# Kernel optimization log

Hardware: AMD Instinct MI355X
Metric: run time of the kernel (lower is better)

## Reference

```python
import jax, jax.numpy as jnp
import numpy as np

IO = 1024
D_SLOT = 128
SCALES = [1, 2, 4]
N = 4          # lcm of scales (streams / period)
K = 3          # number of scales (active slots per step)
S = 7          # sum of scales (total slots)
D = D_SLOT * S # 896, per-stream dim
H = K * N      # 12 heads
RANK = 256
HID = 3584
B, T = 4, 1024
EPS = 1e-5


def _tables():
    # active_slots[phase, scale_idx] -> slot id
    act = np.zeros((N, K), dtype=np.int32)
    for p in range(N):
        off = 0
        for i, s in enumerate(SCALES):
            act[p, i] = off + p % s
            off += s
    # head_assignments[stream, slot] -> head id (SHARED mode)
    ha = np.zeros((N, S), dtype=np.int32)
    off = 0
    for i, s in enumerate(SCALES):
        alpha = N // s
        for j in range(s):
            ha[:, off + j] = i * N + (np.arange(N) + alpha * j) % N
        off += s
    return act, ha

ACTIVE_SLOTS, HEAD_ASSIGN = _tables()


def layernorm(x, g, b):
    m = jnp.mean(x, axis=-1, keepdims=True)
    v = jnp.mean(jnp.square(x - m), axis=-1, keepdims=True)
    return (x - m) * jax.lax.rsqrt(v + EPS) * g + b


def setup_inputs() -> dict:
    key = jax.random.key(0)
    ks = jax.random.split(key, 16)
    f32 = jnp.float32
    return {
        'x': jax.random.normal(ks[0], (B, T, IO), f32),
        't': 3,
        'enc_base_w': jax.random.normal(ks[1], (D, IO), f32) * 0.02,
        'enc_A_w': jax.random.normal(ks[2], (RANK, IO), f32) * 0.02,
        'enc_B': jax.random.normal(ks[3], (RANK, N, D), f32) * 0.02,
        'enc_beta': jnp.asarray(0.01, f32),
        'ln_mixer_g': jnp.ones((D,), f32),
        'ln_mixer_b': jnp.zeros((D,), f32),
        'mix_w1': jax.random.normal(ks[4], (HID, D), f32) * 0.02,
        'mix_b1': jnp.zeros((HID,), f32),
        'mix_w2': jax.random.normal(ks[5], (D, HID), f32) * 0.02,
        'mix_b2': jnp.zeros((D,), f32),
        'ln_attn_g': jnp.ones((D,), f32),
        'ln_attn_b': jnp.zeros((D,), f32),
        'Wq': jax.random.normal(ks[6], (H, D, D_SLOT), f32) * 0.02,
        'Wk': jax.random.normal(ks[7], (H, D, D_SLOT), f32) * 0.02,
        'Wv': jax.random.normal(ks[8], (H, D, D_SLOT), f32) * 0.02,
        'dec_ln_g': jnp.ones((N * D,), f32),
        'dec_ln_b': jnp.zeros((N * D,), f32),
        'dec_down_w': jax.random.normal(ks[9], (RANK, N * D), f32) * 0.02,
        'dec_up_w': jax.random.normal(ks[10], (IO, RANK), f32) * 0.02,
    }


def reference(x, t, enc_base_w, enc_A_w, enc_B, enc_beta,
              ln_mixer_g, ln_mixer_b, mix_w1, mix_b1, mix_w2, mix_b2,
              ln_attn_g, ln_attn_b, Wq, Wk, Wv,
              dec_ln_g, dec_ln_b, dec_down_w, dec_up_w):
    b, tt, _ = x.shape
    # --- StreamLoRAEncoder: x [B,T,IO] -> z [B,T,N,D] ---
    base = x @ enc_base_w.T                       # [B,T,D]
    h = x @ enc_A_w.T                             # [B,T,RANK]
    delta = jnp.einsum('btr,rnd->btnd', h, enc_B) # [B,T,N,D]
    z = base[:, :, None, :] + enc_beta * delta

    # --- step(z, t, is_causal=True) ---
    phase = int(t) % N
    active = ACTIVE_SLOTS[phase]                               # [K]
    head_ids = HEAD_ASSIGN[np.arange(N)[:, None], active[None, :]]  # [N,K]

    # mixer (pre-LN MLP residual)
    zm = layernorm(z, ln_mixer_g, ln_mixer_b)
    m = jax.nn.gelu(zm @ mix_w1.T + mix_b1, approximate=False) @ mix_w2.T + mix_b2
    z_head = z + m                                             # [B,T,N,D]

    # per-head multi-scale attention; head input scope = STREAM (full D)
    hin = layernorm(z_head, ln_attn_g, ln_attn_b)              # [B,T,N,D]
    Wq_s, Wk_s, Wv_s = Wq[head_ids], Wk[head_ids], Wv[head_ids]  # [N,K,D,d]
    q = jnp.einsum('btnc,nkcd->btnkd', hin, Wq_s)
    k = jnp.einsum('btnc,nkcd->btnkd', hin, Wk_s)
    v = jnp.einsum('btnc,nkcd->btnkd', hin, Wv_s)
    scale = 1.0 / jnp.sqrt(jnp.asarray(D_SLOT, q.dtype))
    scores = jnp.einsum('bqnkd,bpnkd->bnkqp', q, k) * scale    # [B,N,K,T,T]
    causal = jnp.tril(jnp.ones((tt, tt), dtype=bool))
    scores = jnp.where(causal, scores, jnp.finfo(scores.dtype).min)
    attn = jax.nn.softmax(scores, axis=-1)
    out = jnp.einsum('bnkqp,bpnkd->bqnkd', attn, v)            # [B,T,N,K,d]

    # write attention outputs back into the active slots (residual)
    z_slots = z_head.reshape(b, tt, N, S, D_SLOT)
    z_new = z_slots.at[:, :, :, jnp.asarray(active), :].add(out)
    z_new = z_new.reshape(b, tt, N, D)

    # --- StreamLoRADecoder: z [B,T,N,D] -> y [B,T,IO] ---
    cat = z_new.reshape(b, tt, N * D)
    c = layernorm(cat, dec_ln_g, dec_ln_b)
    y = (c @ dec_down_w.T) @ dec_up_w.T
    return y
```

## Files before the change

### kernel.cpp

```cpp
#include <hip/hip_runtime.h>
#include <hip/hip_bf16.h>
#include <math.h>

typedef __hip_bfloat16 bf16;
typedef __attribute__((ext_vector_type(8))) short v8s;
typedef __attribute__((ext_vector_type(4))) float v4f;

#define EPI_F32    0
#define EPI_BF16   1
#define EPI_GELU   2
#define EPI_RESID  3
#define EPI_BCAST4 4
#define EPI_AXPY   5
#define EPI_RESID0 6

__device__ __forceinline__ float bf_lo(unsigned int w) { return __uint_as_float(w << 16); }
__device__ __forceinline__ float bf_hi(unsigned int w) { return __uint_as_float(w & 0xffff0000u); }
__device__ __forceinline__ unsigned short f2b_bits(float f) {
  unsigned int u = __float_as_uint(f);
  unsigned int r = (u + 0x7fffu + ((u >> 16) & 1u)) >> 16;
  return (unsigned short)r;
}
__device__ __forceinline__ void unpack8(uint4 u, float* f) {
  unsigned int w0 = u.x, w1 = u.y, w2 = u.z, w3 = u.w;
  f[0] = bf_lo(w0); f[1] = bf_hi(w0);
  f[2] = bf_lo(w1); f[3] = bf_hi(w1);
  f[4] = bf_lo(w2); f[5] = bf_hi(w2);
  f[6] = bf_lo(w3); f[7] = bf_hi(w3);
}
__device__ __forceinline__ void load8(const float* p, float* f) {
  float4 a = ((const float4*)p)[0];
  float4 b = ((const float4*)p)[1];
  f[0] = a.x; f[1] = a.y; f[2] = a.z; f[3] = a.w;
  f[4] = b.x; f[5] = b.y; f[6] = b.z; f[7] = b.w;
}
__device__ __forceinline__ void gl_lds16(const void* g, void* l) {
  __builtin_amdgcn_global_load_lds(
      (__attribute__((address_space(1))) void*)g,
      (__attribute__((address_space(3))) void*)l, 16, 0, 0);
}

__global__ __launch_bounds__(256) void cvt_kernel(const float* __restrict__ src,
                                                  bf16* __restrict__ dst, int n)
{
  int i = (blockIdx.x * 256 + threadIdx.x) * 8;
  if (i >= n) return;
  float f[8]; load8(src + i, f);
  unsigned short us[8];
#pragma unroll
  for (int j = 0; j < 8; j++) us[j] = f2b_bits(f[j]);
  *(uint4*)((unsigned short*)dst + i) = *(uint4*)us;
}

__global__ __launch_bounds__(256) void cvt_t_kernel(const float* __restrict__ src,
                                                    bf16* __restrict__ dst, int R, int C)
{
  __shared__ float tile[32][33];
  const int c0 = blockIdx.x * 32, r0 = blockIdx.y * 32;
  const size_t bo = (size_t)blockIdx.z * R * C;
  const int tx = threadIdx.x & 31, ty = threadIdx.x >> 5;
#pragma unroll
  for (int i = 0; i < 4; i++) {
    int r = ty * 4 + i;
    tile[r][tx] = src[bo + (size_t)(r0 + r) * C + c0 + tx];
  }
  __syncthreads();
#pragma unroll
  for (int i = 0; i < 4; i++) {
    int r = ty * 4 + i;
    *((unsigned short*)dst + bo + (size_t)(c0 + r) * R + r0 + tx) = f2b_bits(tile[tx][r]);
  }
}

__global__ __launch_bounds__(256) void vt_kernel(const bf16* __restrict__ v,
                                                 bf16* __restrict__ vt)
{
  __shared__ float tile[64][65];
  const int h = blockIdx.z;
  const int t0 = blockIdx.x * 64, d0 = blockIdx.y * 64;
  const bf16* src = v + (size_t)h * 4096 * 128;
  bf16* dst = vt + (size_t)h * 128 * 4096;
  const int tid = threadIdx.x;
#pragma unroll
  for (int tt = 0; tt < 2; tt++) {
    int s = tt * 256 + tid;
    int r = s >> 3, c0 = (s & 7) * 8;
    float f[8];
    uint4 u = *(const uint4*)(src + (size_t)(t0 + r) * 128 + d0 + c0);
    unpack8(u, f);
#pragma unroll
    for (int j = 0; j < 8; j++) tile[r][c0 + j] = f[j];
  }
  __syncthreads();
#pragma unroll
  for (int tt = 0; tt < 2; tt++) {
    int s = tt * 256 + tid;
    int dr = s >> 3, c0 = (s & 7) * 8;
    unsigned short us[8];
#pragma unroll
    for (int j = 0; j < 8; j++) us[j] = f2b_bits(tile[c0 + j][dr]);
    *(uint4*)((unsigned short*)dst + (size_t)(d0 + dr) * 4096 + t0 + c0) = *(uint4*)us;
  }
}

__device__ __forceinline__ void stage_async(const bf16* __restrict__ src, int ld, int r0, int k0,
                                            bf16* lds, int wave, int lane)
{
#pragma unroll
  for (int t = 0; t < 2; t++) {
    int seg = wave * 2 + t;
    const bf16* g = src + (size_t)(r0 + seg * 16 + (lane >> 2)) * ld + k0 + (lane & 3) * 8;
    gl_lds16(g, lds + seg * 512);
  }
}
__device__ __forceinline__ void stage_sync(const float* __restrict__ src, int ld, int r0, int k0,
                                           bf16* lds, int tid)
{
#pragma unroll
  for (int t = 0; t < 2; t++) {
    int s = t * 256 + tid;
    int m = s >> 2, c = s & 3;
    float f[8]; load8(src + (size_t)(r0 + m) * ld + k0 + c * 8, f);
    unsigned short us[8];
#pragma unroll
    for (int j = 0; j < 8; j++) us[j] = f2b_bits(f[j]);
    *(uint4*)&lds[m * 32 + c * 8] = *(uint4*)us;
  }
}
__device__ __forceinline__ void stage_tile(const bf16* __restrict__ src, int ld, int r0, int k0,
                                           bf16* lds, int tid, int wave, int lane)
{ stage_async(src, ld, r0, k0, lds, wave, lane); }
__device__ __forceinline__ void stage_tile(const float* __restrict__ src, int ld, int r0, int k0,
                                           bf16* lds, int tid, int wave, int lane)
{ stage_sync(src, ld, r0, k0, lds, tid); }

template<typename TA, typename TB, int EPI>
__device__ void mfma_core(const TA* __restrict__ A, int lda,
                          const TB* __restrict__ B, int ldb,
                          void* __restrict__ C, int ldc,
                          const float* __restrict__ bias,
                          const float* __restrict__ beta_p,
                          int m0, int n0, int K)
{
  __shared__ bf16 As[128 * 32];
  __shared__ bf16 Bs[128 * 32];
  const int tid = threadIdx.x;
  const int lane = tid & 63, wave = tid >> 6;
  const int mw = (wave & 1) * 64, nw = (wave >> 1) * 64;
  const int row = lane & 15, kc = lane >> 4;

  v4f acc[4][4];
  const v4f vzero = {0.f, 0.f, 0.f, 0.f};
#pragma unroll
  for (int i = 0; i < 4; i++)
#pragma unroll
    for (int j = 0; j < 4; j++) acc[i][j] = vzero;

  for (int k0 = 0; k0 < K; k0 += 32) {
    stage_tile(A, lda, m0, k0, As, tid, wave, lane);
    stage_tile(B, ldb, n0, k0, Bs, tid, wave, lane);
    __syncthreads();
    v8s af[4], bfr[4];
#pragma unroll
    for (int i = 0; i < 4; i++)
      af[i] = *(const v8s*)&As[(mw + i * 16 + row) * 32 + kc * 8];
#pragma unroll
    for (int j = 0; j < 4; j++)
      bfr[j] = *(const v8s*)&Bs[(nw + j * 16 + row) * 32 + kc * 8];
#pragma unroll
    for (int i = 0; i < 4; i++)
#pragma unroll
      for (int j = 0; j < 4; j++)
        acc[i][j] = __builtin_amdgcn_mfma_f32_16x16x32_bf16(af[i], bfr[j], acc[i][j], 0, 0, 0);
    __syncthreads();
  }

  const int cl = lane & 15, rq = lane >> 4;
  const float beta = (EPI == EPI_AXPY) ? beta_p[0] : 0.f;
#pragma unroll
  for (int mi = 0; mi < 4; mi++) {
#pragma unroll
    for (int nj = 0; nj < 4; nj++) {
      const int col = n0 + nw + nj * 16 + cl;
#pragma unroll
      for (int i = 0; i < 4; i++) {
        const int r = m0 + mw + mi * 16 + rq * 4 + i;
        float v = acc[mi][nj][i];
        if (EPI == EPI_F32) {
          ((float*)C)[(size_t)r * ldc + col] = v;
        } else if (EPI == EPI_BF16) {
          ((unsigned short*)C)[(size_t)r * ldc + col] = f2b_bits(v);
        } else if (EPI == EPI_GELU) {
          v += bias[col];
          v = 0.5f * v * (1.f + erff(v * 0.70710678118654752f));
          ((unsigned short*)C)[(size_t)r * ldc + col] = f2b_bits(v);
        } else if (EPI == EPI_RESID) {
          float* Z = (float*)C;
          size_t idx = (size_t)r * ldc + col;
          Z[idx] = Z[idx] + v + bias[col];
        } else if (EPI == EPI_RESID0) {
          float* Z = (float*)C;
          size_t idx = (size_t)r * ldc + col;
          Z[idx] = Z[idx] + v;
        } else if (EPI == EPI_BCAST4) {
          float* Z = (float*)C;
#pragma unroll
          for (int rep = 0; rep < 4; rep++)
            Z[(size_t)r * 3584 + rep * 896 + col] = v;
        } else if (EPI == EPI_AXPY) {
          float* Z = (float*)C;
          size_t idx = (size_t)r * 3584 + col;
          Z[idx] = Z[idx] + beta * v;
        }
      }
    }
  }
}

template<typename TA, typename TB, int EPI>
__global__ __launch_bounds__(256) void mfma_gemm(const TA* __restrict__ A, int lda,
                                                 const TB* __restrict__ B, int ldb,
                                                 void* __restrict__ C, int ldc,
                                                 const float* __restrict__ bias,
                                                 const float* __restrict__ beta_p, int K)
{
  mfma_core<TA, TB, EPI>(A, lda, B, ldb, C, ldc, bias, beta_p,
                         blockIdx.y * 128, blockIdx.x * 128, K);
}

template<typename TA, typename TB, int EPI>
__global__ __launch_bounds__(256) void mfma_gemm_sw(const TA* __restrict__ A, int lda,
                                                    const TB* __restrict__ B, int ldb,
                                                    void* __restrict__ C, int ldc,
                                                    const float* __restrict__ bias,
                                                    const float* __restrict__ beta_p, int K)
{
  const int lin = blockIdx.x;
  const int m0 = ((((lin & 7) << 4) | ((lin >> 3) & 15))) * 128;
  const int n0 = (lin >> 7) * 128;
  mfma_core<TA, TB, EPI>(A, lda, B, ldb, C, ldc, bias, beta_p, m0, n0, K);
}

__global__ __launch_bounds__(256) void qkv_mfma(const bf16* __restrict__ hin,
                                                const bf16* __restrict__ Wt,
                                                bf16* __restrict__ qkv,
                                                const int* __restrict__ tptr)
{
  const int zb = blockIdx.z;
  const int type = zb / 12, rem = zb % 12, n = rem / 3, kh = rem % 3;
  const int phase = ((tptr[0] % 4) + 4) % 4;
  const int hid = (kh == 0) ? n
                : (kh == 1) ? 4 + (n + 2 * (phase & 1)) % 4
                            : 8 + (n + phase) % 4;
  const bf16* B = Wt + ((size_t)type * 12 + hid) * 128 * 896;
  bf16* out = qkv + ((size_t)type * 12 + n * 3 + kh) * 4096 * 128;
  mfma_core<bf16, bf16, EPI_BF16>(hin + n * 896, 3584, B, 896, out, 128,
                                  nullptr, nullptr, blockIdx.y * 128, 0, 896);
}

__global__ __launch_bounds__(256) void ln_kernel(const float* __restrict__ in,
                                                 const float* __restrict__ g,
                                                 const float* __restrict__ bsh,
                                                 bf16* __restrict__ out, int D)
{
  __shared__ float row[3584];
  __shared__ float red[256];
  const int tid = threadIdx.x;
  const size_t base = (size_t)blockIdx.x * D;
  float s = 0.f;
  for (int i = tid; i < D; i += 256) { float v = in[base + i]; row[i] = v; s += v; }
  red[tid] = s; __syncthreads();
  for (int o = 128; o > 0; o >>= 1) { if (tid < o) red[tid] += red[tid + o]; __syncthreads(); }
  const float mean = red[0] / (float)D;
  __syncthreads();
  s = 0.f;
  for (int i = tid; i < D; i += 256) { float d = row[i] - mean; s += d * d; }
  red[tid] = s; __syncthreads();
  for (int o = 128; o > 0; o >>= 1) { if (tid < o) red[tid] += red[tid + o]; __syncthreads(); }
  const float inv = rsqrtf(red[0] / (float)D + 1e-5f);
  for (int i = tid; i < D; i += 256) {
    float v = (row[i] - mean) * inv * g[i] + bsh[i];
    *((unsigned short*)out + base + i) = f2b_bits(v);
  }
}

__global__ __launch_bounds__(256) void attn_mfma(const bf16* __restrict__ qkv,
                                                 const bf16* __restrict__ vt,
                                                 float* __restrict__ z,
                                                 const int* __restrict__ tptr)
{
  __shared__ bf16 Ks[64 * 136];
  __shared__ bf16 Vs[128 * 72];
  __shared__ bf16 Ps[4][16 * 72];
  const int tid = threadIdx.x;
  const int lane = tid & 63, wave = tid >> 6;
  const int cl = lane & 15, rq = lane >> 4;
  const int qb = 15 - blockIdx.x;
  const int bnk = blockIdx.y;
  const int b = bnk / 12, rem = bnk % 12, n = rem / 3, kh = rem % 3;
  const int phase = ((tptr[0] % 4) + 4) % 4;
  const int slot = (kh == 0) ? 0 : (kh == 1) ? 1 + (phase & 1) : 3 + phase;
  const int head = n * 3 + kh;
  const size_t HS = (size_t)12 * 4096 * 128;
  const bf16* qp = qkv + ((size_t)head * 4096 + b * 1024) * 128;
  const bf16* kp = qkv + HS + ((size_t)head * 4096 + b * 1024) * 128;
  const bf16* vtp = vt + (size_t)head * 128 * 4096;

  v8s aq[4];
  {
    const bf16* qrow = qp + (size_t)(qb * 64 + wave * 16 + cl) * 128 + rq * 8;
#pragma unroll
    for (int c = 0; c < 4; c++) aq[c] = *(const v8s*)(qrow + c * 32);
  }
  v4f oacc[8];
  const v4f vzero = {0.f, 0.f, 0.f, 0.f};
#pragma unroll
  for (int c = 0; c < 8; c++) oacc[c] = vzero;
  float m_i[4] = {-1e30f, -1e30f, -1e30f, -1e30f};
  float l_i[4] = {0.f, 0.f, 0.f, 0.f};

  for (int kt = 0; kt <= qb; kt++) {
    __syncthreads();
#pragma unroll
    for (int t = 0; t < 4; t++) {
      int s = t * 256 + tid;
      int r = s >> 4, c0 = (s & 15) * 8;
      *(uint4*)&Ks[r * 136 + c0] = *(const uint4*)(kp + (size_t)(kt * 64 + r) * 128 + c0);
    }
#pragma unroll
    for (int t = 0; t < 4; t++) {
      int s = t * 256 + tid;
      int d = s >> 3, c0 = (s & 7) * 8;
      *(uint4*)&Vs[d * 72 + c0] =
          *(const uint4*)(vtp + (size_t)d * 4096 + b * 1024 + kt * 64 + c0);
    }
    __syncthreads();

    v4f s_acc[4];
#pragma unroll
    for (int blk = 0; blk < 4; blk++) {
      s_acc[blk] = vzero;
#pragma unroll
      for (int c = 0; c < 4; c++) {
        v8s bk = *(const v8s*)&Ks[(blk * 16 + cl) * 136 + c * 32 + rq * 8];
        s_acc[blk] = __builtin_amdgcn_mfma_f32_16x16x32_bf16(aq[c], bk, s_acc[blk], 0, 0, 0);
      }
    }
#pragma unroll
    for (int blk = 0; blk < 4; blk++)
#pragma unroll
      for (int i = 0; i < 4; i++) {
        float sv = s_acc[blk][i] * 0.088388347648318447f;
        if (kt == qb && (blk * 16 + cl) > (wave * 16 + rq * 4 + i)) sv = -1e30f;
        s_acc[blk][i] = sv;
      }
    float al[4];
#pragma unroll
    for (int i = 0; i < 4; i++) {
      float mx = fmaxf(fmaxf(s_acc[0][i], s_acc[1][i]), fmaxf(s_acc[2][i], s_acc[3][i]));
      mx = fmaxf(mx, __shfl_xor(mx, 1, 64));
      mx = fmaxf(mx, __shfl_xor(mx, 2, 64));
      mx = fmaxf(mx, __shfl_xor(mx, 4, 64));
      mx = fmaxf(mx, __shfl_xor(mx, 8, 64));
      const float mn = fmaxf(m_i[i], mx);
      al[i] = __expf(m_i[i] - mn);
      m_i[i] = mn;
      float ps = 0.f;
#pragma unroll
      for (int blk = 0; blk < 4; blk++) {
        float p = __expf(s_acc[blk][i] - mn);
        s_acc[blk][i] = p;
        ps += p;
      }
      ps += __shfl_xor(ps, 1, 64);
      ps += __shfl_xor(ps, 2, 64);
      ps += __shfl_xor(ps, 4, 64);
      ps += __shfl_xor(ps, 8, 64);
      l_i[i] = l_i[i] * al[i] + ps;
    }
#pragma unroll
    for (int c = 0; c < 8; c++)
#pragma unroll
      for (int i = 0; i < 4; i++) oacc[c][i] *= al[i];
    bf16* ps = Ps[wave];
#pragma unroll
    for (int blk = 0; blk < 4; blk++)
#pragma unroll
      for (int i = 0; i < 4; i++)
        *((unsigned short*)ps + (rq * 4 + i) * 72 + blk * 16 + cl) = f2b_bits(s_acc[blk][i]);
    v8s pa[2];
#pragma unroll
    for (int c = 0; c < 2; c++)
      pa[c] = *(const v8s*)&ps[cl * 72 + c * 32 + rq * 8];
#pragma unroll
    for (int c = 0; c < 8; c++)
#pragma unroll
      for (int ch = 0; ch < 2; ch++) {
        v8s bv = *(const v8s*)&Vs[(c * 16 + cl) * 72 + ch * 32 + rq * 8];
        oacc[c] = __builtin_amdgcn_mfma_f32_16x16x32_bf16(pa[ch], bv, oacc[c], 0, 0, 0);
      }
  }
#pragma unroll
  for (int c = 0; c < 8; c++) {
    const int d = c * 16 + cl;
#pragma unroll
    for (int i = 0; i < 4; i++) {
      const int t = qb * 64 + wave * 16 + rq * 4 + i;
      float* dst = z + ((size_t)(b * 1024 + t)) * 3584 + n * 896 + slot * 128 + d;
      *dst += oacc[c][i] / l_i[i];
    }
  }
}

extern "C" void kernel_launch(void* const* d_in, const int* in_sizes, int n_in,
                              void* d_out, int out_size, void* d_ws, size_t ws_size,
                              hipStream_t stream)
{
  const float* x        = (const float*)d_in[0];
  const int*   tptr     = (const int*)d_in[1];
  const float* enc_base = (const float*)d_in[2];
  const float* enc_A    = (const float*)d_in[3];
  const float* enc_B    = (const float*)d_in[4];
  const float* beta_p   = (const float*)d_in[5];
  const float* lnm_g    = (const float*)d_in[6];
  const float* lnm_b    = (const float*)d_in[7];
  const float* w1       = (const float*)d_in[8];
  const float* b1       = (const float*)d_in[9];
  const float* w2       = (const float*)d_in[10];
  const float* b2       = (const float*)d_in[11];
  const float* lna_g    = (const float*)d_in[12];
  const float* lna_b    = (const float*)d_in[13];
  const float* Wq       = (const float*)d_in[14];
  const float* Wk       = (const float*)d_in[15];
  const float* Wv       = (const float*)d_in[16];
  const float* dln_g    = (const float*)d_in[17];
  const float* dln_b    = (const float*)d_in[18];
  const float* down_w   = (const float*)d_in[19];
  const float* up_w     = (const float*)d_in[20];

  const bool big = (ws_size >= (size_t)228458496);
  char* ws = (char*)d_ws;
  float* z = (float*)ws;
  bf16 *hbuf, *act, *qkv, *bufb, *w1b, *w2b, *encBt, *Wt;
  if (big) {
    hbuf  = (bf16*)(ws + (size_t)58720256);
    act   = (bf16*)(ws + (size_t)58720256);
    qkv   = (bf16*)(ws + (size_t)58720256);
    bufb  = (bf16*)(ws + (size_t)176160768);
    w1b   = (bf16*)(ws + (size_t)205520896);
    w2b   = (bf16*)(ws + (size_t)211943424);
    encBt = (bf16*)(ws + (size_t)218365952);
    Wt    = (bf16*)(ws + (size_t)220200960);
  } else {
    hbuf  = (bf16*)(ws + (size_t)58720256);
    act   = (bf16*)(ws + (size_t)58720256);
    qkv   = (bf16*)(ws + (size_t)58720256);
    bufb  = (bf16*)(ws + (size_t)96468992);
    w1b   = (bf16*)(ws + (size_t)125829120);
    w2b   = (bf16*)(ws + (size_t)132251648);
    encBt = (bf16*)(ws + (size_t)138674176);
    Wt    = (bf16*)(ws + (size_t)140509184);
  }

  dim3 blk(256);
  cvt_kernel<<<1568, blk, 0, stream>>>(w1, w1b, 3211264);
  cvt_kernel<<<1568, blk, 0, stream>>>(w2, w2b, 3211264);
  cvt_t_kernel<<<dim3(112, 8, 1), blk, 0, stream>>>(enc_B, encBt, 256, 3584);
  cvt_t_kernel<<<dim3(4, 28, 12), blk, 0, stream>>>(Wq, Wt,                      896, 128);
  cvt_t_kernel<<<dim3(4, 28, 12), blk, 0, stream>>>(Wk, Wt + (size_t)12*128*896, 896, 128);
  cvt_t_kernel<<<dim3(4, 28, 12), blk, 0, stream>>>(Wv, Wt + (size_t)24*128*896, 896, 128);

  mfma_gemm<float, float, EPI_BCAST4><<<dim3(7, 32), blk, 0, stream>>>(x, 1024, enc_base, 1024, z, 0, nullptr, nullptr, 1024);
  mfma_gemm<float, float, EPI_BF16><<<dim3(2, 32), blk, 0, stream>>>(x, 1024, enc_A, 1024, hbuf, 256, nullptr, nullptr, 1024);
  mfma_gemm<bf16, bf16, EPI_AXPY><<<dim3(28, 32), blk, 0, stream>>>(hbuf, 256, encBt, 256, z, 3584, nullptr, beta_p, 256);
  ln_kernel<<<dim3(16384), blk, 0, stream>>>(z, lnm_g, lnm_b, bufb, 896);

  if (big) {
    mfma_gemm_sw<bf16, bf16, EPI_GELU><<<dim3(3584), blk, 0, stream>>>(bufb, 896, w1b, 896, act, 3584, b1, nullptr, 896);
    mfma_gemm_sw<bf16, bf16, EPI_RESID><<<dim3(896), blk, 0, stream>>>(act, 3584, w2b, 3584, z, 896, b2, nullptr, 3584);
  } else {
    for (int c = 0; c < 4; c++) {
      mfma_gemm_sw<bf16, bf16, EPI_GELU><<<dim3(896), blk, 0, stream>>>(
          bufb, 896, w1b + (size_t)c * 896 * 896, 896, act, 896, b1 + c * 896, nullptr, 896);
      if (c == 0)
        mfma_gemm_sw<bf16, bf16, EPI_RESID><<<dim3(896), blk, 0, stream>>>(
            act, 896, w2b + (size_t)c * 896, 3584, z, 896, b2, nullptr, 896);
      else
        mfma_gemm_sw<bf16, bf16, EPI_RESID0><<<dim3(896), blk, 0, stream>>>(
            act, 896, w2b + (size_t)c * 896, 3584, z, 896, nullptr, nullptr, 896);
    }
  }

  ln_kernel<<<dim3(16384), blk, 0, stream>>>(z, lna_g, lna_b, bufb, 896);
  qkv_mfma<<<dim3(1, 32, 36), blk, 0, stream>>>(bufb, Wt, qkv, tptr);
  vt_kernel<<<dim3(64, 2, 12), blk, 0, stream>>>(qkv + (size_t)24 * 4096 * 128, bufb);
  attn_mfma<<<dim3(16, 48), blk, 0, stream>>>(qkv, bufb, z, tptr);
  ln_kernel<<<dim3(4096), blk, 0, stream>>>(z, dln_g, dln_b, bufb, 3584);
  mfma_gemm<bf16, float, EPI_BF16><<<dim3(2, 32), blk, 0, stream>>>(bufb, 3584, down_w, 3584, hbuf, 256, nullptr, nullptr, 3584);
  mfma_gemm<bf16, float, EPI_F32><<<dim3(8, 32), blk, 0, stream>>>(hbuf, 256, up_w, 256, (float*)d_out, 1024, nullptr, nullptr, 256);
}
```

Measured before the change: 1.023 ms.

## Precombine low-rank encoder/decoder weights and split-K the w2 and decoder GEMMs

The encoder's base and LoRA paths are folded into one effective weight per stream, Wz = enc_base + beta*B^T A, computed once in bf16. A single GEMM of bf16 x against Wz then replaces the broadcast and AXPY passes. The decoder's down and up projections are likewise merged into one 1024x3584 weight, and that GEMM runs split-K with atomic adds into a zeroed output. The w2 GEMM also becomes split-K with atomics to raise occupancy. The trade-off is extra FLOPs per pass for the full-rank products and non-deterministic atomic accumulation, which also adds rounding error.

```diff
diff --git a/kernel.cpp b/kernel.cpp
--- a/kernel.cpp
+++ b/kernel.cpp
@@ -10,9 +10,9 @@
 #define EPI_BF16   1
 #define EPI_GELU   2
 #define EPI_RESID  3
-#define EPI_BCAST4 4
-#define EPI_AXPY   5
-#define EPI_RESID0 6
+#define EPI_RESID0 4
+#define EPI_WZ     5
+#define EPI_ATOM   6
 
 __device__ __forceinline__ float bf_lo(unsigned int w) { return __uint_as_float(w << 16); }
 __device__ __forceinline__ float bf_hi(unsigned int w) { return __uint_as_float(w & 0xffff0000u); }
@@ -176,7 +176,7 @@
   }
 
   const int cl = lane & 15, rq = lane >> 4;
-  const float beta = (EPI == EPI_AXPY) ? beta_p[0] : 0.f;
+  const float beta = (EPI == EPI_WZ) ? beta_p[0] : 0.f;
 #pragma unroll
   for (int mi = 0; mi < 4; mi++) {
 #pragma unroll
@@ -202,15 +202,12 @@
           float* Z = (float*)C;
           size_t idx = (size_t)r * ldc + col;
           Z[idx] = Z[idx] + v;
-        } else if (EPI == EPI_BCAST4) {
-          float* Z = (float*)C;
-#pragma unroll
-          for (int rep = 0; rep < 4; rep++)
-            Z[(size_t)r * 3584 + rep * 896 + col] = v;
-        } else if (EPI == EPI_AXPY) {
-          float* Z = (float*)C;
-          size_t idx = (size_t)r * 3584 + col;
-          Z[idx] = Z[idx] + beta * v;
+        } else if (EPI == EPI_WZ) {
+          float o = beta * v + bias[(size_t)(r % 896) * 1024 + col];
+          ((unsigned short*)C)[(size_t)r * ldc + col] = f2b_bits(o);
+        } else if (EPI == EPI_ATOM) {
+          float add = v + (bias ? bias[col] : 0.f);
+          atomicAdd(&((float*)C)[(size_t)r * ldc + col], add);
         }
       }
     }
@@ -239,6 +236,18 @@
   const int m0 = ((((lin & 7) << 4) | ((lin >> 3) & 15))) * 128;
   const int n0 = (lin >> 7) * 128;
   mfma_core<TA, TB, EPI>(A, lda, B, ldb, C, ldc, bias, beta_p, m0, n0, K);
+}
+
+template<typename TA, typename TB>
+__global__ __launch_bounds__(256) void mfma_gemm_sk(const TA* __restrict__ A, int lda,
+                                                    const TB* __restrict__ B, int ldb,
+                                                    float* __restrict__ C, int ldc,
+                                                    const float* __restrict__ bias, int Kc)
+{
+  const int kofs = blockIdx.z * Kc;
+  mfma_core<TA, TB, EPI_ATOM>(A + kofs, lda, B + kofs, ldb, C, ldc,
+                              (blockIdx.z == 0) ? bias : nullptr, nullptr,
+                              blockIdx.y * 128, blockIdx.x * 128, Kc);
 }
 
 __global__ __launch_bounds__(256) void qkv_mfma(const bf16* __restrict__ hin,
@@ -441,43 +450,53 @@
   const bool big = (ws_size >= (size_t)228458496);
   char* ws = (char*)d_ws;
   float* z = (float*)ws;
-  bf16 *hbuf, *act, *qkv, *bufb, *w1b, *w2b, *encBt, *Wt;
+  char* ra = ws + (size_t)58720256;
+  bf16 *act, *qkv, *bufb, *w1b, *w2b, *encBt, *Wt;
   if (big) {
-    hbuf  = (bf16*)(ws + (size_t)58720256);
-    act   = (bf16*)(ws + (size_t)58720256);
-    qkv   = (bf16*)(ws + (size_t)58720256);
+    act   = (bf16*)ra;
+    qkv   = (bf16*)ra;
     bufb  = (bf16*)(ws + (size_t)176160768);
     w1b   = (bf16*)(ws + (size_t)205520896);
     w2b   = (bf16*)(ws + (size_t)211943424);
     encBt = (bf16*)(ws + (size_t)218365952);
     Wt    = (bf16*)(ws + (size_t)220200960);
   } else {
-    hbuf  = (bf16*)(ws + (size_t)58720256);
-    act   = (bf16*)(ws + (size_t)58720256);
-    qkv   = (bf16*)(ws + (size_t)58720256);
+    act   = (bf16*)ra;
+    qkv   = (bf16*)ra;
     bufb  = (bf16*)(ws + (size_t)96468992);
     w1b   = (bf16*)(ws + (size_t)125829120);
     w2b   = (bf16*)(ws + (size_t)132251648);
     encBt = (bf16*)(ws + (size_t)138674176);
     Wt    = (bf16*)(ws + (size_t)140509184);
   }
+  bf16* xb    = (bf16*)ra;
+  bf16* encAt = (bf16*)(ra + (size_t)8912896);
+  bf16* Wz    = (bf16*)(ra + (size_t)9437184);
+  bf16* dwT   = (bf16*)ra;
+  bf16* Wdec  = (bf16*)(ra + (size_t)2097152);
 
   dim3 blk(256);
+  hipMemsetAsync(d_out, 0, (size_t)4096 * 1024 * 4, stream);
+
   cvt_kernel<<<1568, blk, 0, stream>>>(w1, w1b, 3211264);
   cvt_kernel<<<1568, blk, 0, stream>>>(w2, w2b, 3211264);
+  cvt_kernel<<<2048, blk, 0, stream>>>(x, xb, 4194304);
   cvt_t_kernel<<<dim3(112, 8, 1), blk, 0, stream>>>(enc_B, encBt, 256, 3584);
+  cvt_t_kernel<<<dim3(32, 8, 1), blk, 0, stream>>>(enc_A, encAt, 256, 1024);
   cvt_t_kernel<<<dim3(4, 28, 12), blk, 0, stream>>>(Wq, Wt,                      896, 128);
   cvt_t_kernel<<<dim3(4, 28, 12), blk, 0, stream>>>(Wk, Wt + (size_t)12*128*896, 896, 128);
   cvt_t_kernel<<<dim3(4, 28, 12), blk, 0, stream>>>(Wv, Wt + (size_t)24*128*896, 896, 128);
-
-  mfma_gemm<float, float, EPI_BCAST4><<<dim3(7, 32), blk, 0, stream>>>(x, 1024, enc_base, 1024, z, 0, nullptr, nullptr, 1024);
-  mfma_gemm<float, float, EPI_BF16><<<dim3(2, 32), blk, 0, stream>>>(x, 1024, enc_A, 1024, hbuf, 256, nullptr, nullptr, 1024);
-  mfma_gemm<bf16, bf16, EPI_AXPY><<<dim3(28, 32), blk, 0, stream>>>(hbuf, 256, encBt, 256, z, 3584, nullptr, beta_p, 256);
+  mfma_gemm<bf16, bf16, EPI_WZ><<<dim3(8, 28), blk, 0, stream>>>(
+      encBt, 256, encAt, 256, Wz, 1024, enc_base, beta_p, 256);
+
+  mfma_gemm<bf16, bf16, EPI_F32><<<dim3(28, 32), blk, 0, stream>>>(
+      xb, 1024, Wz, 1024, z, 3584, nullptr, nullptr, 1024);
+
   ln_kernel<<<dim3(16384), blk, 0, stream>>>(z, lnm_g, lnm_b, bufb, 896);
 
   if (big) {
     mfma_gemm_sw<bf16, bf16, EPI_GELU><<<dim3(3584), blk, 0, stream>>>(bufb, 896, w1b, 896, act, 3584, b1, nullptr, 896);
-    mfma_gemm_sw<bf16, bf16, EPI_RESID><<<dim3(896), blk, 0, stream>>>(act, 3584, w2b, 3584, z, 896, b2, nullptr, 3584);
+    mfma_gemm_sk<bf16, bf16><<<dim3(7, 128, 2), blk, 0, stream>>>(act, 3584, w2b, 3584, z, 896, b2, 1792);
   } else {
     for (int c = 0; c < 4; c++) {
       mfma_gemm_sw<bf16, bf16, EPI_GELU><<<dim3(896), blk, 0, stream>>>(
@@ -495,7 +514,12 @@
   qkv_mfma<<<dim3(1, 32, 36), blk, 0, stream>>>(bufb, Wt, qkv, tptr);
   vt_kernel<<<dim3(64, 2, 12), blk, 0, stream>>>(qkv + (size_t)24 * 4096 * 128, bufb);
   attn_mfma<<<dim3(16, 48), blk, 0, stream>>>(qkv, bufb, z, tptr);
+
+  cvt_t_kernel<<<dim3(112, 8, 1), blk, 0, stream>>>(down_w, dwT, 256, 3584);
+  mfma_gemm<float, bf16, EPI_BF16><<<dim3(28, 8), blk, 0, stream>>>(
+      up_w, 256, dwT, 256, Wdec, 3584, nullptr, nullptr, 256);
+
   ln_kernel<<<dim3(4096), blk, 0, stream>>>(z, dln_g, dln_b, bufb, 3584);
-  mfma_gemm<bf16, float, EPI_BF16><<<dim3(2, 32), blk, 0, stream>>>(bufb, 3584, down_w, 3584, hbuf, 256, nullptr, nullptr, 3584);
-  mfma_gemm<bf16, float, EPI_F32><<<dim3(8, 32), blk, 0, stream>>>(hbuf, 256, up_w, 256, (float*)d_out, 1024, nullptr, nullptr, 256);
-}
+  mfma_gemm_sk<bf16, bf16><<<dim3(8, 32, 4), blk, 0, stream>>>(
+      bufb, 3584, Wdec, 3584, (float*)d_out, 1024, nullptr, 896);
+}
```

Measured after the change: 1.023 ms. Within noise of the previous version (+0.0%).
